# Kernel optimization log

Measured on AMD Instinct MI355X. Metric: run time of the kernel, lower is better.

The kernel has to match this reference:

```python
import jax, jax.numpy as jnp
import numpy as np

B, S, D, H = 4, 2048, 1024, 16
DK = D // H  # 64


def setup_inputs() -> dict:
    key = jax.random.key(0)
    ks = jax.random.split(key, 5)
    scale = 1.0 / np.sqrt(D)
    return {
        "embeddings": jax.random.normal(ks[0], (B, S, D), dtype=jnp.float32),
        "W_q": jax.random.normal(ks[1], (D, D), dtype=jnp.float32) * scale,
        "W_k": jax.random.normal(ks[2], (D, D), dtype=jnp.float32) * scale,
        "W_v": jax.random.normal(ks[3], (D, D), dtype=jnp.float32) * scale,
        "W_o": jax.random.normal(ks[4], (D, D), dtype=jnp.float32) * scale,
    }


def reference(embeddings, W_q, W_k, W_v, W_o):
    # torch nn.Linear: y = x @ W.T  (weights are [out, in])
    b, s, d = embeddings.shape
    h, dk = H, DK
    q = embeddings @ W_q.T  # [b, s, d]
    k = embeddings @ W_k.T
    v = embeddings @ W_v.T
    # split heads along last dim (matches the per-head slicing in the torch loop)
    q = q.reshape(b, s, h, dk)
    k = k.reshape(b, s, h, dk)
    v = v.reshape(b, s, h, dk)
    scores = jnp.einsum("bqhd,bkhd->bhqk", q, k) / jnp.sqrt(jnp.float32(dk))
    p = jax.nn.softmax(scores, axis=-1)  # dropout is identity at eval
    ctx = jnp.einsum("bhqk,bkhd->bqhd", p, v).reshape(b, s, d)
    return ctx @ W_o.T
```

## Files before the change

kernel.cpp:

```cpp
#include <hip/hip_runtime.h>
#include <hip/hip_bf16.h>

typedef unsigned short u16;
typedef __attribute__((ext_vector_type(8))) short bf16x8;
typedef __attribute__((ext_vector_type(4))) float f32x4;
typedef __attribute__((ext_vector_type(2))) unsigned int u32x2;

#define AS1 __attribute__((address_space(1)))
#define AS3 __attribute__((address_space(3)))

constexpr int Bc = 4, Sc = 2048, Dc = 1024, Hc = 16, DKc = 64;
constexpr size_t EDc = (size_t)Bc * Sc * Dc;
constexpr size_t WDc = (size_t)Dc * Dc;

__device__ __forceinline__ void g2l16(const void* g, void* l) {
  __builtin_amdgcn_global_load_lds((const AS1 unsigned int*)g,
                                   (AS3 unsigned int*)l, 16, 0, 0);
}

__device__ __forceinline__ u16 f2b(float f) {
  union { float f; unsigned u; } x; x.f = f;
  unsigned r = x.u + 0x7fffu + ((x.u >> 16) & 1u);
  return (u16)(r >> 16);
}

#if __has_builtin(__builtin_amdgcn_cvt_pk_bf16_f32)
typedef __attribute__((ext_vector_type(2))) __bf16 hbf2;
__device__ __forceinline__ unsigned f2b_pk(float a, float b) {
  union { hbf2 v; unsigned u; } x;
  x.v = __builtin_amdgcn_cvt_pk_bf16_f32(a, b);
  return x.u;
}
#else
__device__ __forceinline__ unsigned f2b_pk(float a, float b) {
  return (unsigned)f2b(a) | ((unsigned)f2b(b) << 16);
}
#endif

__device__ __forceinline__ float fast_exp2(float x) {
#if __has_builtin(__builtin_amdgcn_exp2f)
  return __builtin_amdgcn_exp2f(x);
#else
  return exp2f(x);
#endif
}

__global__ __launch_bounds__(256)
void cvt_all(const float* __restrict__ e, const float* __restrict__ wq,
             const float* __restrict__ wk, const float* __restrict__ wv,
             const float* __restrict__ wo, u16* __restrict__ dst) {
  int bx = blockIdx.x;
  const float* src;
  size_t doff;
  int chunk;
  if (bx < 4096) {
    src = e; doff = 0; chunk = bx;
  } else {
    int t = bx - 4096;
    int w = t >> 9;
    chunk = t & 511;
    src = (w == 0) ? wq : (w == 1) ? wk : (w == 2) ? wv : wo;
    doff = EDc + (size_t)w * WDc;
  }
  size_t i = ((size_t)chunk * 256 + threadIdx.x) * 8;
  float4 a = *(const float4*)(src + i);
  float4 b = *(const float4*)(src + i + 4);
  bf16x8 o;
  o[0] = (short)f2b(a.x); o[1] = (short)f2b(a.y);
  o[2] = (short)f2b(a.z); o[3] = (short)f2b(a.w);
  o[4] = (short)f2b(b.x); o[5] = (short)f2b(b.y);
  o[6] = (short)f2b(b.z); o[7] = (short)f2b(b.w);
  *(bf16x8*)(dst + doff + i) = o;
}

__global__ __launch_bounds__(256, 2)
void gemm_qkv(const u16* __restrict__ X, const u16* __restrict__ Wq,
              const u16* __restrict__ Wk, const u16* __restrict__ Wv,
              u16* __restrict__ Qo, u16* __restrict__ Ko,
              u16* __restrict__ VTo) {
  constexpr int BM = 128, BK = 64, K = Dc, N = Dc;
  __shared__ u16 As[BM * BK];
  __shared__ u16 Bs[BM * BK];

  const int tid = threadIdx.x;
  const int wave = tid >> 6, lane = tid & 63;
  const int mr = lane & 15, quad = lane >> 4, mr7 = lane & 7;
  const int sect = blockIdx.x >> 3;
  const int n0 = (blockIdx.x & 7) * 128;
  const int m0 = blockIdx.y * BM;
  const u16* W = (sect == 0) ? Wq : (sect == 1) ? Wk : Wv;
  const int wm = (wave >> 1) * 64, wn = (wave & 1) * 64;
  const int ldr = lane >> 3;
  const int ldc_sw = ((lane & 7) ^ (ldr & 7)) * 8;

  const f32x4 zero = {0.f, 0.f, 0.f, 0.f};
  f32x4 acc[4][4];
  #pragma unroll
  for (int i = 0; i < 4; i++)
    #pragma unroll
    for (int j = 0; j < 4; j++) acc[i][j] = zero;

  for (int k0 = 0; k0 < K; k0 += BK) {
    __syncthreads();
    #pragma unroll
    for (int i = 0; i < 4; i++) {
      int row = wave * 32 + i * 8;
      g2l16(X + (size_t)(m0 + row + ldr) * K + k0 + ldc_sw, As + row * BK);
      g2l16(W + (size_t)(n0 + row + ldr) * K + k0 + ldc_sw, Bs + row * BK);
    }
    __syncthreads();

    #pragma unroll
    for (int c = 0; c < 2; c++) {
      bf16x8 a[4], b[4];
      #pragma unroll
      for (int i = 0; i < 4; i++)
        a[i] = *(const bf16x8*)(As + (wm + i * 16 + mr) * BK +
                                (((c * 4 + quad) ^ mr7) * 8));
      #pragma unroll
      for (int j = 0; j < 4; j++)
        b[j] = *(const bf16x8*)(Bs + (wn + j * 16 + mr) * BK +
                                (((c * 4 + quad) ^ mr7) * 8));
      #pragma unroll
      for (int i = 0; i < 4; i++)
        #pragma unroll
        for (int j = 0; j < 4; j++)
          acc[i][j] = __builtin_amdgcn_mfma_f32_16x16x32_bf16(
              a[i], b[j], acc[i][j], 0, 0, 0);
    }
  }

  if (sect == 2) {
    #pragma unroll
    for (int i = 0; i < 4; i++)
      #pragma unroll
      for (int j = 0; j < 4; j++) {
        int mbase = m0 + wm + i * 16 + quad * 4;
        int n = n0 + wn + j * 16 + mr;
        int b = mbase >> 11, s = mbase & 2047;
        int h = n >> 6, d = n & 63;
        ushort4 pk;
        pk.x = f2b(acc[i][j][0]); pk.y = f2b(acc[i][j][1]);
        pk.z = f2b(acc[i][j][2]); pk.w = f2b(acc[i][j][3]);
        *(ushort4*)(VTo + ((size_t)((b * Hc + h) * DKc + d)) * Sc + s) = pk;
      }
  } else {
    const float scale = (sect == 0) ? 0.18033688f : 1.0f;
    u16* Y = (sect == 0) ? Qo : Ko;
    #pragma unroll
    for (int i = 0; i < 4; i++)
      #pragma unroll
      for (int j = 0; j < 4; j++)
        #pragma unroll
        for (int r = 0; r < 4; r++) {
          int m = m0 + wm + i * 16 + quad * 4 + r;
          int n = n0 + wn + j * 16 + mr;
          Y[(size_t)m * N + n] = f2b(acc[i][j][r] * scale);
        }
  }
}

__global__ __launch_bounds__(256, 2)
void gemm_out(const u16* __restrict__ X, const u16* __restrict__ W,
              float* __restrict__ Y, int M, int N, int K) {
  constexpr int BM = 128, BK = 64;
  __shared__ u16 As[BM * BK];
  __shared__ u16 Bs[BM * BK];

  const int tid = threadIdx.x;
  const int wave = tid >> 6, lane = tid & 63;
  const int mr = lane & 15, quad = lane >> 4, mr7 = lane & 7;
  const int m0 = blockIdx.y * BM, n0 = blockIdx.x * BM;
  const int wm = (wave >> 1) * 64, wn = (wave & 1) * 64;
  const int ldr = lane >> 3;
  const int ldc_sw = ((lane & 7) ^ (ldr & 7)) * 8;

  const f32x4 zero = {0.f, 0.f, 0.f, 0.f};
  f32x4 acc[4][4];
  #pragma unroll
  for (int i = 0; i < 4; i++)
    #pragma unroll
    for (int j = 0; j < 4; j++) acc[i][j] = zero;

  for (int k0 = 0; k0 < K; k0 += BK) {
    __syncthreads();
    #pragma unroll
    for (int i = 0; i < 4; i++) {
      int row = wave * 32 + i * 8;
      g2l16(X + (size_t)(m0 + row + ldr) * K + k0 + ldc_sw, As + row * BK);
      g2l16(W + (size_t)(n0 + row + ldr) * K + k0 + ldc_sw, Bs + row * BK);
    }
    __syncthreads();

    #pragma unroll
    for (int c = 0; c < 2; c++) {
      bf16x8 a[4], b[4];
      #pragma unroll
      for (int i = 0; i < 4; i++)
        a[i] = *(const bf16x8*)(As + (wm + i * 16 + mr) * BK +
                                (((c * 4 + quad) ^ mr7) * 8));
      #pragma unroll
      for (int j = 0; j < 4; j++)
        b[j] = *(const bf16x8*)(Bs + (wn + j * 16 + mr) * BK +
                                (((c * 4 + quad) ^ mr7) * 8));
      #pragma unroll
      for (int i = 0; i < 4; i++)
        #pragma unroll
        for (int j = 0; j < 4; j++)
          acc[i][j] = __builtin_amdgcn_mfma_f32_16x16x32_bf16(
              a[i], b[j], acc[i][j], 0, 0, 0);
    }
  }

  #pragma unroll
  for (int i = 0; i < 4; i++)
    #pragma unroll
    for (int j = 0; j < 4; j++)
      #pragma unroll
      for (int r = 0; r < 4; r++) {
        int m = m0 + wm + i * 16 + quad * 4 + r;
        int n = n0 + wn + j * 16 + mr;
        Y[(size_t)m * N + n] = acc[i][j][r];
      }
}

__global__ __launch_bounds__(256, 4)
void attn(const u16* __restrict__ Q, const u16* __restrict__ K,
          const u16* __restrict__ VT, u16* __restrict__ O) {
  __shared__ u16 Ks[64 * 64];
  __shared__ u16 Vs[64 * 64];
  __shared__ u16 Ps[4][16 * 64];

  const int tid = threadIdx.x;
  const int wave = tid >> 6, lane = tid & 63;
  const int mr = lane & 15, quad = lane >> 4, mr7 = lane & 7;
  const int bh = blockIdx.y;
  const int b = bh >> 4, h = bh & 15;
  const int q0 = blockIdx.x * 128;
  const size_t headK = (size_t)b * Sc * Dc + (size_t)h * DKc;
  const size_t headV = (size_t)bh * DKc * Sc;
  const int ldr = lane >> 3;
  const int ldc_sw = ((lane & 7) ^ (ldr & 7)) * 8;

  bf16x8 qa[2][2];
  #pragma unroll
  for (int t = 0; t < 2; t++)
    #pragma unroll
    for (int c = 0; c < 2; c++)
      qa[t][c] = *(const bf16x8*)(Q + headK +
          (size_t)(q0 + wave * 32 + t * 16 + mr) * Dc + c * 32 + quad * 8);

  const f32x4 zero = {0.f, 0.f, 0.f, 0.f};
  f32x4 o[2][4];
  float lrow[2][4];
  #pragma unroll
  for (int t = 0; t < 2; t++)
    #pragma unroll
    for (int i = 0; i < 4; i++) {
      o[t][i] = zero;
      lrow[t][i] = 0.f;
    }

  u16* Pw = Ps[wave];

  for (int kt = 0; kt < Sc / 64; kt++) {
    const int k0 = kt * 64;
    __syncthreads();
    #pragma unroll
    for (int i = 0; i < 2; i++) {
      int row0 = wave * 16 + i * 8;
      int p = row0 + ldr;
      int srow = ((p & 15) << 2) | (p >> 4);
      g2l16(K + headK + (size_t)(k0 + srow) * Dc + ldc_sw, Ks + row0 * 64);
      g2l16(VT + headV + (size_t)(row0 + ldr) * Sc + k0 + ldc_sw, Vs + row0 * 64);
    }
    __syncthreads();

    f32x4 s0[4], s1[4];
    #pragma unroll
    for (int kc = 0; kc < 4; kc++) {
      s0[kc] = zero; s1[kc] = zero;
      #pragma unroll
      for (int c = 0; c < 2; c++) {
        bf16x8 kb = *(const bf16x8*)(Ks + (kc * 16 + mr) * 64 +
                                     (((c * 4 + quad) ^ mr7) * 8));
        s0[kc] = __builtin_amdgcn_mfma_f32_16x16x32_bf16(qa[0][c], kb, s0[kc], 0, 0, 0);
        s1[kc] = __builtin_amdgcn_mfma_f32_16x16x32_bf16(qa[1][c], kb, s1[kc], 0, 0, 0);
      }
    }

    bf16x8 pa[2][2];
    #pragma unroll
    for (int t = 0; t < 2; t++) {
      f32x4* s = t ? s1 : s0;
      float* lR = lrow[t];
      #pragma unroll
      for (int r = 0; r < 4; r++) {
        float p0 = fast_exp2(fminf(s[0][r], 100.f));
        float p1 = fast_exp2(fminf(s[1][r], 100.f));
        float p2 = fast_exp2(fminf(s[2][r], 100.f));
        float p3 = fast_exp2(fminf(s[3][r], 100.f));
        lR[r] += (p0 + p1) + (p2 + p3);
        u32x2 w;
        w.x = f2b_pk(p0, p1);
        w.y = f2b_pk(p2, p3);
        *(u32x2*)(Pw + (quad * 4 + r) * 64 + mr * 4) = w;
      }
      #pragma unroll
      for (int c = 0; c < 2; c++)
        pa[t][c] = *(const bf16x8*)(Pw + mr * 64 + c * 32 + quad * 8);
    }

    #pragma unroll
    for (int ni = 0; ni < 4; ni++)
      #pragma unroll
      for (int c = 0; c < 2; c++) {
        bf16x8 vb = *(const bf16x8*)(Vs + (ni * 16 + mr) * 64 +
                                     (((c * 4 + quad) ^ mr7) * 8));
        o[0][ni] = __builtin_amdgcn_mfma_f32_16x16x32_bf16(pa[0][c], vb, o[0][ni], 0, 0, 0);
        o[1][ni] = __builtin_amdgcn_mfma_f32_16x16x32_bf16(pa[1][c], vb, o[1][ni], 0, 0, 0);
      }
  }

  #pragma unroll
  for (int t = 0; t < 2; t++)
    #pragma unroll
    for (int r = 0; r < 4; r++) {
      float l = lrow[t][r];
      #pragma unroll
      for (int off = 1; off < 16; off <<= 1)
        l += __shfl_xor(l, off, 64);
      float inv = 1.0f / l;
      #pragma unroll
      for (int ni = 0; ni < 4; ni++) {
        int qq = q0 + wave * 32 + t * 16 + quad * 4 + r;
        O[headK + (size_t)qq * Dc + ni * 16 + mr] = f2b(o[t][ni][r] * inv);
      }
    }
}

extern "C" void kernel_launch(void* const* d_in, const int* in_sizes, int n_in,
                              void* d_out, int out_size, void* d_ws, size_t ws_size,
                              hipStream_t stream) {
  const float* emb = (const float*)d_in[0];
  const float* Wq  = (const float*)d_in[1];
  const float* Wk  = (const float*)d_in[2];
  const float* Wv  = (const float*)d_in[3];
  const float* Wo  = (const float*)d_in[4];
  float* out = (float*)d_out;

  const int M = Bc * Sc;

  u16* Eb  = (u16*)d_ws;
  u16* Wqb = Eb  + EDc;
  u16* Wkb = Wqb + WDc;
  u16* Wvb = Wkb + WDc;
  u16* Wob = Wvb + WDc;
  u16* Qb  = Wob + WDc;
  u16* Kb  = Qb  + EDc;
  u16* VTb = Kb  + EDc;
  u16* Cb  = Qb;

  dim3 blk(256);
  cvt_all<<<dim3(4096 + 4 * 512), blk, 0, stream>>>(emb, Wq, Wk, Wv, Wo, Eb);

  gemm_qkv<<<dim3(24, M / 128), blk, 0, stream>>>(Eb, Wqb, Wkb, Wvb,
                                                  Qb, Kb, VTb);

  attn<<<dim3(Sc / 128, Bc * Hc), blk, 0, stream>>>(Qb, Kb, VTb, Cb);

  gemm_out<<<dim3(Dc / 128, M / 128), blk, 0, stream>>>(Cb, Wob, out,
                                                        M, Dc, Dc);
}
```

Measured before the change: 299.1 us.

## Double-buffer attention K/V tiles, compute row sums via MFMA, transpose V epilogue

The attention kernel now double-buffers K and V tiles in LDS, prefetching the next tile while computing on the current one, which cuts one barrier per iteration. Softmax row sums are now computed with an MFMA against a vector of ones instead of scalar adds and a cross-lane shuffle reduction. The fminf clamp on scores is dropped. In the QKV GEMM the V section swaps MFMA operands so its transposed store writes along the sequence dimension, trading vector stores for scalar ones. Doubling the K/V LDS buffers raises shared memory per block, which may limit occupancy.

```diff
diff --git a/kernel.cpp b/kernel.cpp
--- a/kernel.cpp
+++ b/kernel.cpp
@@ -92,6 +92,7 @@
   const int wm = (wave >> 1) * 64, wn = (wave & 1) * 64;
   const int ldr = lane >> 3;
   const int ldc_sw = ((lane & 7) ^ (ldr & 7)) * 8;
+  const bool vsec = (sect == 2);
 
   const f32x4 zero = {0.f, 0.f, 0.f, 0.f};
   f32x4 acc[4][4];
@@ -121,29 +122,40 @@
       for (int j = 0; j < 4; j++)
         b[j] = *(const bf16x8*)(Bs + (wn + j * 16 + mr) * BK +
                                 (((c * 4 + quad) ^ mr7) * 8));
-      #pragma unroll
-      for (int i = 0; i < 4; i++)
+      if (vsec) {
         #pragma unroll
-        for (int j = 0; j < 4; j++)
-          acc[i][j] = __builtin_amdgcn_mfma_f32_16x16x32_bf16(
-              a[i], b[j], acc[i][j], 0, 0, 0);
-    }
-  }
-
-  if (sect == 2) {
-    #pragma unroll
-    for (int i = 0; i < 4; i++)
+        for (int i = 0; i < 4; i++)
+          #pragma unroll
+          for (int j = 0; j < 4; j++)
+            acc[i][j] = __builtin_amdgcn_mfma_f32_16x16x32_bf16(
+                b[j], a[i], acc[i][j], 0, 0, 0);
+      } else {
+        #pragma unroll
+        for (int i = 0; i < 4; i++)
+          #pragma unroll
+          for (int j = 0; j < 4; j++)
+            acc[i][j] = __builtin_amdgcn_mfma_f32_16x16x32_bf16(
+                a[i], b[j], acc[i][j], 0, 0, 0);
+      }
+    }
+  }
+
+  if (vsec) {
+    #pragma unroll
+    for (int i = 0; i < 4; i++) {
+      int s_glob = m0 + wm + i * 16 + mr;
+      int bb = s_glob >> 11, s = s_glob & 2047;
       #pragma unroll
       for (int j = 0; j < 4; j++) {
-        int mbase = m0 + wm + i * 16 + quad * 4;
-        int n = n0 + wn + j * 16 + mr;
-        int b = mbase >> 11, s = mbase & 2047;
-        int h = n >> 6, d = n & 63;
-        ushort4 pk;
-        pk.x = f2b(acc[i][j][0]); pk.y = f2b(acc[i][j][1]);
-        pk.z = f2b(acc[i][j][2]); pk.w = f2b(acc[i][j][3]);
-        *(ushort4*)(VTo + ((size_t)((b * Hc + h) * DKc + d)) * Sc + s) = pk;
-      }
+        int nbase = n0 + wn + j * 16 + quad * 4;
+        #pragma unroll
+        for (int r = 0; r < 4; r++) {
+          int n = nbase + r;
+          int h = n >> 6, d = n & 63;
+          VTo[((size_t)((bb * Hc + h) * DKc + d)) * Sc + s] = f2b(acc[i][j][r]);
+        }
+      }
+    }
   } else {
     const float scale = (sect == 0) ? 0.18033688f : 1.0f;
     u16* Y = (sect == 0) ? Qo : Ko;
@@ -227,8 +239,8 @@
 __global__ __launch_bounds__(256, 4)
 void attn(const u16* __restrict__ Q, const u16* __restrict__ K,
           const u16* __restrict__ VT, u16* __restrict__ O) {
-  __shared__ u16 Ks[64 * 64];
-  __shared__ u16 Vs[64 * 64];
+  __shared__ u16 Ks[2][64 * 64];
+  __shared__ u16 Vs[2][64 * 64];
   __shared__ u16 Ps[4][16 * 64];
 
   const int tid = threadIdx.x;
@@ -242,6 +254,11 @@
   const int ldr = lane >> 3;
   const int ldc_sw = ((lane & 7) ^ (ldr & 7)) * 8;
 
+  const int row0a = wave * 16, row0b = wave * 16 + 8;
+  const int pa_r = row0a + ldr, pb_r = row0b + ldr;
+  const int sra = ((pa_r & 15) << 2) | (pa_r >> 4);
+  const int srb = ((pb_r & 15) << 2) | (pb_r >> 4);
+
   bf16x8 qa[2][2];
   #pragma unroll
   for (int t = 0; t < 2; t++)
@@ -250,31 +267,42 @@
       qa[t][c] = *(const bf16x8*)(Q + headK +
           (size_t)(q0 + wave * 32 + t * 16 + mr) * Dc + c * 32 + quad * 8);
 
+  bf16x8 ones;
+  #pragma unroll
+  for (int j = 0; j < 8; j++) ones[j] = (short)0x3F80;
+
   const f32x4 zero = {0.f, 0.f, 0.f, 0.f};
   f32x4 o[2][4];
-  float lrow[2][4];
-  #pragma unroll
-  for (int t = 0; t < 2; t++)
-    #pragma unroll
-    for (int i = 0; i < 4; i++) {
-      o[t][i] = zero;
-      lrow[t][i] = 0.f;
-    }
+  f32x4 ol[2];
+  #pragma unroll
+  for (int t = 0; t < 2; t++) {
+    ol[t] = zero;
+    #pragma unroll
+    for (int i = 0; i < 4; i++) o[t][i] = zero;
+  }
 
   u16* Pw = Ps[wave];
 
+  {
+    const u16* Kb_ = K + headK;
+    const u16* Vb_ = VT + headV;
+    g2l16(Kb_ + (size_t)sra * Dc + ldc_sw, Ks[0] + row0a * 64);
+    g2l16(Kb_ + (size_t)srb * Dc + ldc_sw, Ks[0] + row0b * 64);
+    g2l16(Vb_ + (size_t)(row0a + ldr) * Sc + ldc_sw, Vs[0] + row0a * 64);
+    g2l16(Vb_ + (size_t)(row0b + ldr) * Sc + ldc_sw, Vs[0] + row0b * 64);
+  }
+  __syncthreads();
+
   for (int kt = 0; kt < Sc / 64; kt++) {
-    const int k0 = kt * 64;
-    __syncthreads();
-    #pragma unroll
-    for (int i = 0; i < 2; i++) {
-      int row0 = wave * 16 + i * 8;
-      int p = row0 + ldr;
-      int srow = ((p & 15) << 2) | (p >> 4);
-      g2l16(K + headK + (size_t)(k0 + srow) * Dc + ldc_sw, Ks + row0 * 64);
-      g2l16(VT + headV + (size_t)(row0 + ldr) * Sc + k0 + ldc_sw, Vs + row0 * 64);
-    }
-    __syncthreads();
+    const int cur = kt & 1;
+    if (kt + 1 < Sc / 64) {
+      const int nk0 = (kt + 1) * 64;
+      const int nxt = cur ^ 1;
+      g2l16(K + headK + (size_t)(nk0 + sra) * Dc + ldc_sw, Ks[nxt] + row0a * 64);
+      g2l16(K + headK + (size_t)(nk0 + srb) * Dc + ldc_sw, Ks[nxt] + row0b * 64);
+      g2l16(VT + headV + (size_t)(row0a + ldr) * Sc + nk0 + ldc_sw, Vs[nxt] + row0a * 64);
+      g2l16(VT + headV + (size_t)(row0b + ldr) * Sc + nk0 + ldc_sw, Vs[nxt] + row0b * 64);
+    }
 
     f32x4 s0[4], s1[4];
     #pragma unroll
@@ -282,7 +310,7 @@
       s0[kc] = zero; s1[kc] = zero;
       #pragma unroll
       for (int c = 0; c < 2; c++) {
-        bf16x8 kb = *(const bf16x8*)(Ks + (kc * 16 + mr) * 64 +
+        bf16x8 kb = *(const bf16x8*)(Ks[cur] + (kc * 16 + mr) * 64 +
                                      (((c * 4 + quad) ^ mr7) * 8));
         s0[kc] = __builtin_amdgcn_mfma_f32_16x16x32_bf16(qa[0][c], kb, s0[kc], 0, 0, 0);
         s1[kc] = __builtin_amdgcn_mfma_f32_16x16x32_bf16(qa[1][c], kb, s1[kc], 0, 0, 0);
@@ -293,14 +321,12 @@
     #pragma unroll
     for (int t = 0; t < 2; t++) {
       f32x4* s = t ? s1 : s0;
-      float* lR = lrow[t];
       #pragma unroll
       for (int r = 0; r < 4; r++) {
-        float p0 = fast_exp2(fminf(s[0][r], 100.f));
-        float p1 = fast_exp2(fminf(s[1][r], 100.f));
-        float p2 = fast_exp2(fminf(s[2][r], 100.f));
-        float p3 = fast_exp2(fminf(s[3][r], 100.f));
-        lR[r] += (p0 + p1) + (p2 + p3);
+        float p0 = fast_exp2(s[0][r]);
+        float p1 = fast_exp2(s[1][r]);
+        float p2 = fast_exp2(s[2][r]);
+        float p3 = fast_exp2(s[3][r]);
         u32x2 w;
         w.x = f2b_pk(p0, p1);
         w.y = f2b_pk(p2, p3);
@@ -309,28 +335,29 @@
       #pragma unroll
       for (int c = 0; c < 2; c++)
         pa[t][c] = *(const bf16x8*)(Pw + mr * 64 + c * 32 + quad * 8);
+      #pragma unroll
+      for (int c = 0; c < 2; c++)
+        ol[t] = __builtin_amdgcn_mfma_f32_16x16x32_bf16(pa[t][c], ones, ol[t], 0, 0, 0);
     }
 
     #pragma unroll
     for (int ni = 0; ni < 4; ni++)
       #pragma unroll
       for (int c = 0; c < 2; c++) {
-        bf16x8 vb = *(const bf16x8*)(Vs + (ni * 16 + mr) * 64 +
+        bf16x8 vb = *(const bf16x8*)(Vs[cur] + (ni * 16 + mr) * 64 +
                                      (((c * 4 + quad) ^ mr7) * 8));
         o[0][ni] = __builtin_amdgcn_mfma_f32_16x16x32_bf16(pa[0][c], vb, o[0][ni], 0, 0, 0);
         o[1][ni] = __builtin_amdgcn_mfma_f32_16x16x32_bf16(pa[1][c], vb, o[1][ni], 0, 0, 0);
       }
+
+    __syncthreads();
   }
 
   #pragma unroll
   for (int t = 0; t < 2; t++)
     #pragma unroll
     for (int r = 0; r < 4; r++) {
-      float l = lrow[t][r];
-      #pragma unroll
-      for (int off = 1; off < 16; off <<= 1)
-        l += __shfl_xor(l, off, 64);
-      float inv = 1.0f / l;
+      float inv = 1.0f / ol[t][r];
       #pragma unroll
       for (int ni = 0; ni < 4; ni++) {
         int qq = q0 + wave * 32 + t * 16 + quad * 4 + r;
```

Measured after the change: 274.6 us. 8.2% less time.
